# Optimization experiments

Measured on AMD Instinct MI355X. Metric: run time of the kernel, lower is better.

## Reference

```python
import jax, jax.numpy as jnp
import numpy as np

B, L, E, H = 1, 2048, 1024, 16
D = E // H
SCALE = D ** -0.5


def rotary(x):
    # x: [b, h, L, d]; ESM-style rotary over the sequence axis
    d = x.shape[-1]
    inv_freq = 1.0 / (10000.0 ** (jnp.arange(0, d, 2, dtype=jnp.float32) / d))
    t = jnp.arange(x.shape[-2], dtype=jnp.float32)
    freqs = t[:, None] * inv_freq[None, :]            # [L, d/2]
    emb = jnp.concatenate([freqs, freqs], axis=-1)    # [L, d]
    cos, sin = jnp.cos(emb), jnp.sin(emb)
    x1, x2 = jnp.split(x, 2, axis=-1)
    rot = jnp.concatenate([-x2, x1], axis=-1)
    return x * cos + rot * sin


def setup_inputs() -> dict:
    key = jax.random.key(0)
    ks = jax.random.split(key, 12)
    s = 0.02
    return {
        "query": jax.random.normal(ks[0], (B, L, E), jnp.float32),
        "key_padding_mask": jnp.zeros((B, L), dtype=bool),
        "is_same_entity": jax.random.randint(ks[1], (B, L, L), 0, 2),
        "has_same_sequence": jax.random.randint(ks[2], (B, L, L), 0, 2),
        "Wq": jax.random.normal(ks[3], (E, E), jnp.float32) * s,
        "bq": jnp.zeros((E,), jnp.float32),
        "Wk": jax.random.normal(ks[4], (E, E), jnp.float32) * s,
        "bk": jnp.zeros((E,), jnp.float32),
        "Wv": jax.random.normal(ks[5], (E, E), jnp.float32) * s,
        "bv": jnp.zeros((E,), jnp.float32),
        "Wo": jax.random.normal(ks[6], (E, E), jnp.float32) * s,
        "bo": jnp.zeros((E,), jnp.float32),
        "ent_emb": jax.random.normal(ks[7], (2, H), jnp.float32) * s,
        "seq_emb": jax.random.normal(ks[8], (2, H), jnp.float32) * s,
    }


def reference(query, key_padding_mask, is_same_entity, has_same_sequence,
              Wq, bq, Wk, bk, Wv, bv, Wo, bo, ent_emb, seq_emb):
    b, l, e = query.shape
    h, d = H, e // H

    def proj(W, bias):
        y = jnp.einsum('ble,fe->blf', query, W) + bias
        return y.reshape(b, l, h, d).transpose(0, 2, 1, 3)  # [b,h,L,d]

    q = proj(Wq, bq) * SCALE
    k = proj(Wk, bk)
    v = proj(Wv, bv)

    # pre-rotary (raw) attention weights
    attn_raw = jnp.einsum('bhid,bhjd->bhij', q, k)
    q_r, k_r = rotary(q), rotary(k)
    attn = jnp.einsum('bhid,bhjd->bhij', q_r, k_r)

    # blend: use rotary weights within same sequence, mean-shifted raw elsewhere
    hss = has_same_sequence.astype(bool)[:, None, :, :]  # [b,1,L,L]
    attn_diff = jax.lax.stop_gradient(jnp.mean(attn - attn_raw, axis=(2, 3)))  # [b,h]
    attn_raw = attn_raw + attn_diff[:, :, None, None]
    w = jnp.where(hss, attn, attn_raw)

    # learned entity/sequence positional bias
    pos = ent_emb[is_same_entity] + seq_emb[has_same_sequence]  # [b,L,L,h]
    w = w + jnp.transpose(pos, (0, 3, 1, 2))

    w = jnp.where(key_padding_mask[:, None, None, :], -jnp.inf, w)
    a = jax.nn.softmax(w, axis=-1)

    o = jnp.einsum('bhij,bhjd->bhid', a, v)
    o = o.transpose(0, 2, 1, 3).reshape(b, l, e)
    return jnp.einsum('ble,fe->blf', o, Wo) + bo
```

## Files before the change

### kernel.cpp

```cpp
#include <hip/hip_runtime.h>
#include <math.h>

constexpr int L = 2048;
constexpr int E = 1024;
constexpr int H = 16;
constexpr int D = 64;
constexpr float ATT_SCALE = 0.125f;

typedef __attribute__((ext_vector_type(8))) short short8;
typedef __attribute__((ext_vector_type(4))) float f32x4;

__device__ inline unsigned short cvt_bf16(float x) {
  unsigned int u = __builtin_bit_cast(unsigned int, x);
  unsigned int r = u + 0x7fffu + ((u >> 16) & 1u);
  return (unsigned short)(r >> 16);
}
__device__ inline short8 ld8(const unsigned short* p) {
  return *reinterpret_cast<const short8*>(p);
}

__global__ __launch_bounds__(256) void rope_table_k(float* __restrict__ cos_t,
                                                    float* __restrict__ sin_t) {
  int idx = blockIdx.x * 256 + threadIdx.x;
  if (idx >= L * 32) return;
  int l = idx >> 5, m = idx & 31;
  double invf = exp(-(double)m * (log(10000.0) / 32.0));
  double ph = (double)l * invf;
  cos_t[idx] = (float)cos(ph);
  sin_t[idx] = (float)sin(ph);
}

__global__ __launch_bounds__(256) void cvt_all_k(
    const float* __restrict__ q, const float* __restrict__ wq,
    const float* __restrict__ wk, const float* __restrict__ wv,
    const float* __restrict__ wo, unsigned short* __restrict__ dst) {
  int idx = blockIdx.x * 256 + threadIdx.x;
  const float* src;
  int local;
  if (idx < 262144)      { src = q;  local = idx; }
  else if (idx < 393216) { src = wq; local = idx - 262144; }
  else if (idx < 524288) { src = wk; local = idx - 393216; }
  else if (idx < 655360) { src = wv; local = idx - 524288; }
  else                   { src = wo; local = idx - 655360; }
  const float4* s = (const float4*)src + (size_t)local * 2;
  float4 a = s[0], b = s[1];
  short8 o;
  o[0] = cvt_bf16(a.x); o[1] = cvt_bf16(a.y); o[2] = cvt_bf16(a.z); o[3] = cvt_bf16(a.w);
  o[4] = cvt_bf16(b.x); o[5] = cvt_bf16(b.y); o[6] = cvt_bf16(b.z); o[7] = cvt_bf16(b.w);
  *(short8*)&dst[(size_t)idx * 8] = o;
}

__global__ __launch_bounds__(256) void mask_pack_k(const int* __restrict__ hss,
                                                   const int* __restrict__ ise,
                                                   unsigned char* __restrict__ mbf) {
  int idx = blockIdx.x * 256 + threadIdx.x;
  int i = idx >> 9;
  int rem = idx & 511;
  int jt = rem >> 4, lr = rem & 15;
  size_t rb = (size_t)i * 2048 + jt * 64 + lr;
  unsigned int out = 0;
#pragma unroll
  for (int c = 0; c < 4; ++c) {
    unsigned int hv = (unsigned)hss[rb + c * 16] & 1u;
    unsigned int ev = (unsigned)ise[rb + c * 16] & 1u;
    out |= (hv | (ev << 1)) << (8 * c);
  }
  *(unsigned int*)&mbf[(size_t)i * 2048 + jt * 64 + lr * 4] = out;
}

__global__ __launch_bounds__(256) void proj_qkv(
    const unsigned short* __restrict__ Xb,
    const unsigned short* __restrict__ wqb, const unsigned short* __restrict__ wkb,
    const unsigned short* __restrict__ wvb,
    const float* __restrict__ bq, const float* __restrict__ bk,
    const float* __restrict__ bv,
    float* __restrict__ qf, float* __restrict__ kf, float* __restrict__ vf) {
  int by = blockIdx.y;
  int sel = by >> 4;
  int col0 = (by & 15) * 64;
  int row0 = blockIdx.x * 64;
  const unsigned short* Wb = (sel == 0) ? wqb : (sel == 1) ? wkb : wvb;
  const float* bias = (sel == 0) ? bq : (sel == 1) ? bk : bv;
  float scale = (sel == 0) ? ATT_SCALE : 1.0f;
  float* Y = (sel == 0) ? qf : (sel == 1) ? kf : vf;

  int tid = threadIdx.x;
  int w = tid >> 6, lane = tid & 63, lr = lane & 15, lg = lane >> 4;
  int wm = w >> 1, wn = w & 1;

  f32x4 acc[2][2];
#pragma unroll
  for (int m = 0; m < 2; ++m)
#pragma unroll
    for (int n = 0; n < 2; ++n) acc[m][n] = f32x4{0.f, 0.f, 0.f, 0.f};

  const unsigned short* xa[2];
  const unsigned short* wb2[2];
#pragma unroll
  for (int m = 0; m < 2; ++m)
    xa[m] = Xb + (size_t)(row0 + wm * 32 + m * 16 + lr) * 1024 + lg * 8;
#pragma unroll
  for (int n = 0; n < 2; ++n)
    wb2[n] = Wb + (size_t)(col0 + wn * 32 + n * 16 + lr) * 1024 + lg * 8;

#pragma unroll 2
  for (int k0 = 0; k0 < 1024; k0 += 64) {
    short8 a[2][2], b[2][2];
#pragma unroll
    for (int m = 0; m < 2; ++m) {
      a[m][0] = ld8(xa[m] + k0);
      a[m][1] = ld8(xa[m] + k0 + 32);
    }
#pragma unroll
    for (int n = 0; n < 2; ++n) {
      b[n][0] = ld8(wb2[n] + k0);
      b[n][1] = ld8(wb2[n] + k0 + 32);
    }
#pragma unroll
    for (int m = 0; m < 2; ++m)
#pragma unroll
      for (int n = 0; n < 2; ++n) {
        acc[m][n] = __builtin_amdgcn_mfma_f32_16x16x32_bf16(a[m][0], b[n][0], acc[m][n], 0, 0, 0);
        acc[m][n] = __builtin_amdgcn_mfma_f32_16x16x32_bf16(a[m][1], b[n][1], acc[m][n], 0, 0, 0);
      }
  }

#pragma unroll
  for (int m = 0; m < 2; ++m)
#pragma unroll
    for (int n = 0; n < 2; ++n) {
      int f = col0 + wn * 32 + n * 16 + lr;
      float bvv = bias[f];
#pragma unroll
      for (int rr = 0; rr < 4; ++rr) {
        int row = row0 + wm * 32 + m * 16 + lg * 4 + rr;
        Y[((size_t)(f >> 6) * L + row) * 64 + (f & 63)] = (acc[m][n][rr] + bvv) * scale;
      }
    }
}

__global__ __launch_bounds__(256) void proj_o(
    const unsigned short* __restrict__ Xb, const unsigned short* __restrict__ Wb,
    const float* __restrict__ bias, float* __restrict__ out) {
  int col0 = blockIdx.y * 64;
  int row0 = blockIdx.x * 64;
  int tid = threadIdx.x;
  int w = tid >> 6, lane = tid & 63, lr = lane & 15, lg = lane >> 4;
  int wm = w >> 1, wn = w & 1;

  f32x4 acc[2][2];
#pragma unroll
  for (int m = 0; m < 2; ++m)
#pragma unroll
    for (int n = 0; n < 2; ++n) acc[m][n] = f32x4{0.f, 0.f, 0.f, 0.f};

  const unsigned short* xa[2];
  const unsigned short* wb2[2];
#pragma unroll
  for (int m = 0; m < 2; ++m)
    xa[m] = Xb + (size_t)(row0 + wm * 32 + m * 16 + lr) * 1024 + lg * 8;
#pragma unroll
  for (int n = 0; n < 2; ++n)
    wb2[n] = Wb + (size_t)(col0 + wn * 32 + n * 16 + lr) * 1024 + lg * 8;

#pragma unroll 2
  for (int k0 = 0; k0 < 1024; k0 += 64) {
    short8 a[2][2], b[2][2];
#pragma unroll
    for (int m = 0; m < 2; ++m) {
      a[m][0] = ld8(xa[m] + k0);
      a[m][1] = ld8(xa[m] + k0 + 32);
    }
#pragma unroll
    for (int n = 0; n < 2; ++n) {
      b[n][0] = ld8(wb2[n] + k0);
      b[n][1] = ld8(wb2[n] + k0 + 32);
    }
#pragma unroll
    for (int m = 0; m < 2; ++m)
#pragma unroll
      for (int n = 0; n < 2; ++n) {
        acc[m][n] = __builtin_amdgcn_mfma_f32_16x16x32_bf16(a[m][0], b[n][0], acc[m][n], 0, 0, 0);
        acc[m][n] = __builtin_amdgcn_mfma_f32_16x16x32_bf16(a[m][1], b[n][1], acc[m][n], 0, 0, 0);
      }
  }

#pragma unroll
  for (int m = 0; m < 2; ++m)
#pragma unroll
    for (int n = 0; n < 2; ++n) {
      int f = col0 + wn * 32 + n * 16 + lr;
      float bvv = bias[f];
#pragma unroll
      for (int rr = 0; rr < 4; ++rr) {
        int row = row0 + wm * 32 + m * 16 + lg * 4 + rr;
        out[(size_t)row * 1024 + f] = acc[m][n][rr] + bvv;
      }
    }
}

__global__ __launch_bounds__(256) void postproc_k(
    const float* __restrict__ q, const float* __restrict__ k,
    unsigned short* __restrict__ qb, unsigned short* __restrict__ qrb,
    unsigned short* __restrict__ kb, unsigned short* __restrict__ krb,
    const float* __restrict__ cos_t, const float* __restrict__ sin_t,
    float* __restrict__ sums) {
  int h = blockIdx.x;
  int lc = blockIdx.y;
  int t = threadIdx.x;
  int d = t & 63, lq = t >> 6;
  int m = d & 31;
  float sign = (d < 32) ? -1.0f : 1.0f;
  float sq = 0.f, sk = 0.f, sqr = 0.f, skr = 0.f;
#pragma unroll 4
  for (int i = 0; i < 16; ++i) {
    int l = lc * 64 + i * 4 + lq;
    size_t base = ((size_t)h * L + l) * 64 + d;
    float cv = cos_t[l * 32 + m], sv = sin_t[l * 32 + m];
    float qv = q[base];
    float qp = __shfl_xor(qv, 32);
    float qrv = qv * cv + sign * qp * sv;
    float kv = k[base];
    float kp = __shfl_xor(kv, 32);
    float krv = kv * cv + sign * kp * sv;
    qb[base] = cvt_bf16(qv);
    qrb[base] = cvt_bf16(qrv);
    kb[base] = cvt_bf16(kv);
    krb[base] = cvt_bf16(krv);
    sq += qv; sk += kv; sqr += qrv; skr += krv;
  }
  __shared__ float red[256];
  float vals[4] = {sq, sk, sqr, skr};
#pragma unroll
  for (int a = 0; a < 4; ++a) {
    red[t] = vals[a];
    __syncthreads();
    if (lq == 0) {
      float tot = red[d] + red[d + 64] + red[d + 128] + red[d + 192];
      atomicAdd(&sums[((size_t)a * H + h) * D + d], tot);
    }
    __syncthreads();
  }
}

__global__ __launch_bounds__(256) void vt_k(const float* __restrict__ v,
                                            unsigned short* __restrict__ vtb) {
  __shared__ float tile[64][65];
  int h = blockIdx.x, lt = blockIdx.y, t = threadIdx.x;
  int row = t >> 2, cq = (t & 3) * 16;
  const float* src = v + ((size_t)h * L + lt * 64 + row) * 64 + cq;
#pragma unroll
  for (int x = 0; x < 4; ++x) {
    float4 a = *(const float4*)&src[x * 4];
    tile[row][cq + x * 4 + 0] = a.x;
    tile[row][cq + x * 4 + 1] = a.y;
    tile[row][cq + x * 4 + 2] = a.z;
    tile[row][cq + x * 4 + 3] = a.w;
  }
  __syncthreads();
  int dcol = t >> 2, lq = (t & 3) * 16;
  short8 o0, o1;
#pragma unroll
  for (int x = 0; x < 8; ++x) o0[x] = cvt_bf16(tile[lq + x][dcol]);
#pragma unroll
  for (int x = 0; x < 8; ++x) o1[x] = cvt_bf16(tile[lq + 8 + x][dcol]);
  unsigned short* dst = vtb + ((size_t)h * 64 + dcol) * L + lt * 64 + lq;
  *(short8*)dst = o0;
  *(short8*)(dst + 8) = o1;
}

__global__ void diff_k(const float* __restrict__ sums, float* __restrict__ diffp) {
  int h = threadIdx.x;
  if (h < H) {
    const float* sq  = sums + (0 * H + h) * D;
    const float* sk  = sums + (1 * H + h) * D;
    const float* sqr = sums + (2 * H + h) * D;
    const float* skr = sums + (3 * H + h) * D;
    float a = 0.f, b = 0.f;
    for (int d = 0; d < D; ++d) { a += sqr[d] * skr[d]; b += sq[d] * sk[d]; }
    diffp[h] = (a - b) / ((float)L * (float)L);
  }
}

__global__ __launch_bounds__(256) void attn_mfma(
    const unsigned short* __restrict__ qb, const unsigned short* __restrict__ qrb,
    const unsigned short* __restrict__ kb, const unsigned short* __restrict__ krb,
    const unsigned short* __restrict__ vtb, const unsigned char* __restrict__ mbf,
    const float* __restrict__ diffp, const float* __restrict__ ent,
    const float* __restrict__ seq, float* __restrict__ opart,
    float* __restrict__ mpart, float* __restrict__ lpart) {
  __shared__ char p_s[8192];

  int bid = blockIdx.x;
  int xcd = bid & 7, g = bid >> 3;
  int h = xcd * 2 + (g >> 6);
  int sub = g & 63;
  int it = sub & 31, js = sub >> 5;
  int i0 = it * 64;
  int j0base = js * 1024;

  int tid = threadIdx.x;
  int w = tid >> 6, lane = tid & 63, lr = lane & 15, lg = lane >> 4;

  const size_t hb = (size_t)h * L * 64;
  const unsigned short* qh = qb + hb;
  const unsigned short* qrh = qrb + hb;
  const unsigned short* kh = kb + hb;
  const unsigned short* krh = krb + hb;
  const unsigned short* vth = vtb + hb;

  short8 aq[2], aqr[2];
  {
    size_t qbase = (size_t)(i0 + w * 16 + lr) * 64 + lg * 8;
    aq[0] = ld8(qh + qbase);
    aq[1] = ld8(qh + qbase + 32);
    aqr[0] = ld8(qrh + qbase);
    aqr[1] = ld8(qrh + qbase + 32);
  }

  float e0 = ent[h], de = ent[H + h] - e0;
  float s0b = seq[h], dsb = seq[H + h] - s0b;
  float base_b = e0 + s0b;
  float dh = diffp[h];

  float m_r[4], l_r[4];
  f32x4 oacc[4];
#pragma unroll
  for (int rr = 0; rr < 4; ++rr) { m_r[rr] = -INFINITY; l_r[rr] = 0.f; }
#pragma unroll
  for (int n = 0; n < 4; ++n) oacc[n] = f32x4{0.f, 0.f, 0.f, 0.f};

  int koff[4];
#pragma unroll
  for (int c = 0; c < 4; ++c) koff[c] = (c * 16 + lr) * 64 + lg * 8;
  size_t vtoff[4];
#pragma unroll
  for (int n = 0; n < 4; ++n) vtoff[n] = (size_t)(n * 16 + lr) * L + lg * 8;
  int prd0 = w * 2048 + lr * 128 + ((lg * 16) ^ ((lr & 7) << 4));
  int prd1 = w * 2048 + lr * 128 + ((64 + lg * 16) ^ ((lr & 7) << 4));
  size_t mrow0 = (size_t)(i0 + w * 16 + lg * 4) * 2048 + lr * 4;

  for (int jt = 0; jt < 16; ++jt) {
    int j0 = j0base + jt * 64;
    int jb = j0 * 64;

    f32x4 sraw[4], srot[4];
#pragma unroll
    for (int c = 0; c < 4; ++c) {
      sraw[c] = f32x4{0.f, 0.f, 0.f, 0.f};
      srot[c] = f32x4{0.f, 0.f, 0.f, 0.f};
    }
#pragma unroll
    for (int c = 0; c < 4; ++c) {
      short8 b0 = ld8(kh + jb + koff[c]);
      short8 b1 = ld8(kh + jb + koff[c] + 32);
      sraw[c] = __builtin_amdgcn_mfma_f32_16x16x32_bf16(aq[0], b0, sraw[c], 0, 0, 0);
      sraw[c] = __builtin_amdgcn_mfma_f32_16x16x32_bf16(aq[1], b1, sraw[c], 0, 0, 0);
      short8 r0 = ld8(krh + jb + koff[c]);
      short8 r1 = ld8(krh + jb + koff[c] + 32);
      srot[c] = __builtin_amdgcn_mfma_f32_16x16x32_bf16(aqr[0], r0, srot[c], 0, 0, 0);
      srot[c] = __builtin_amdgcn_mfma_f32_16x16x32_bf16(aqr[1], r1, srot[c], 0, 0, 0);
    }

    unsigned int mw[4];
#pragma unroll
    for (int rr = 0; rr < 4; ++rr)
      mw[rr] = *(const unsigned int*)(mbf + mrow0 + (size_t)rr * 2048 + j0);

#pragma unroll
    for (int rr = 0; rr < 4; ++rr) {
      float sv[4];
#pragma unroll
      for (int c = 0; c < 4; ++c) {
        unsigned int b = (mw[rr] >> (8 * c)) & 0xffu;
        float srv = sraw[c][rr] + dh;
        float sov = srot[c][rr];
        float s = ((b & 1) ? sov : srv) + base_b + ((b & 1) ? dsb : 0.f) + ((b & 2) ? de : 0.f);
        sv[c] = s;
      }
      float tmax = fmaxf(fmaxf(sv[0], sv[1]), fmaxf(sv[2], sv[3]));
#pragma unroll
      for (int off = 1; off <= 8; off <<= 1) tmax = fmaxf(tmax, __shfl_xor(tmax, off));
      float mnew = fmaxf(m_r[rr], tmax);
      float corr = __expf(m_r[rr] - mnew);
      float p[4];
      float psum = 0.f;
#pragma unroll
      for (int c = 0; c < 4; ++c) { p[c] = __expf(sv[c] - mnew); psum += p[c]; }
#pragma unroll
      for (int off = 1; off <= 8; off <<= 1) psum += __shfl_xor(psum, off);
      l_r[rr] = l_r[rr] * corr + psum;
      m_r[rr] = mnew;
#pragma unroll
      for (int n = 0; n < 4; ++n) oacc[n][rr] *= corr;
      int prow = lg * 4 + rr;
      int pb = w * 2048 + prow * 128;
      int sw = (prow & 7) << 4;
#pragma unroll
      for (int c = 0; c < 4; ++c)
        *(unsigned short*)(p_s + pb + (((c * 16 + lr) * 2) ^ sw)) = cvt_bf16(p[c]);
    }

    short8 pa0 = *(const short8*)(p_s + prd0);
    short8 pa1 = *(const short8*)(p_s + prd1);
#pragma unroll
    for (int n = 0; n < 4; ++n) {
      short8 v0 = ld8(vth + vtoff[n] + j0);
      short8 v1 = ld8(vth + vtoff[n] + j0 + 32);
      oacc[n] = __builtin_amdgcn_mfma_f32_16x16x32_bf16(pa0, v0, oacc[n], 0, 0, 0);
      oacc[n] = __builtin_amdgcn_mfma_f32_16x16x32_bf16(pa1, v1, oacc[n], 0, 0, 0);
    }
  }

#pragma unroll
  for (int rr = 0; rr < 4; ++rr) {
    int row = i0 + w * 16 + lg * 4 + rr;
    size_t pr = (size_t)(js * 16 + h) * L + row;
    size_t obase = pr * 64;
#pragma unroll
    for (int n = 0; n < 4; ++n) opart[obase + n * 16 + lr] = oacc[n][rr];
    if (lr == 0) {
      mpart[pr] = m_r[rr];
      lpart[pr] = l_r[rr];
    }
  }
}

__global__ __launch_bounds__(256) void combine_k(
    const float* __restrict__ opart, const float* __restrict__ mpart,
    const float* __restrict__ lpart, unsigned short* __restrict__ obf) {
  int idx = blockIdx.x * 256 + threadIdx.x;
  int c8 = idx & 7;
  int row = (idx >> 3) & 2047;
  int h = idx >> 14;
  size_t r0 = (size_t)h * L + row;
  size_t r1 = (size_t)(16 + h) * L + row;
  float m0 = mpart[r0], m1 = mpart[r1];
  float mm = fmaxf(m0, m1);
  float c0 = __expf(m0 - mm), c1 = __expf(m1 - mm);
  float inv = 1.0f / (lpart[r0] * c0 + lpart[r1] * c1);
  float s0 = c0 * inv, s1 = c1 * inv;
  const float4* p0 = (const float4*)&opart[r0 * 64 + c8 * 8];
  const float4* p1 = (const float4*)&opart[r1 * 64 + c8 * 8];
  float4 a0 = p0[0], a1 = p0[1], b0 = p1[0], b1 = p1[1];
  short8 o;
  o[0] = cvt_bf16(a0.x * s0 + b0.x * s1);
  o[1] = cvt_bf16(a0.y * s0 + b0.y * s1);
  o[2] = cvt_bf16(a0.z * s0 + b0.z * s1);
  o[3] = cvt_bf16(a0.w * s0 + b0.w * s1);
  o[4] = cvt_bf16(a1.x * s0 + b1.x * s1);
  o[5] = cvt_bf16(a1.y * s0 + b1.y * s1);
  o[6] = cvt_bf16(a1.z * s0 + b1.z * s1);
  o[7] = cvt_bf16(a1.w * s0 + b1.w * s1);
  *(short8*)&obf[(size_t)row * 1024 + h * 64 + c8 * 8] = o;
}

extern "C" void kernel_launch(void* const* d_in, const int* in_sizes, int n_in,
                              void* d_out, int out_size, void* d_ws, size_t ws_size,
                              hipStream_t stream) {
  (void)in_sizes; (void)n_in; (void)out_size; (void)ws_size;
  const float* query = (const float*)d_in[0];
  const int* ise = (const int*)d_in[2];
  const int* hss = (const int*)d_in[3];
  const float* Wq = (const float*)d_in[4];
  const float* bq = (const float*)d_in[5];
  const float* Wk = (const float*)d_in[6];
  const float* bk = (const float*)d_in[7];
  const float* Wv = (const float*)d_in[8];
  const float* bv = (const float*)d_in[9];
  const float* Wo = (const float*)d_in[10];
  const float* bo = (const float*)d_in[11];
  const float* ent = (const float*)d_in[12];
  const float* seq = (const float*)d_in[13];
  float* out = (float*)d_out;

  const size_t MQ = (size_t)L * E;
  const size_t MW = (size_t)E * E;

  float* ws = (float*)d_ws;
  float* qf = ws;
  float* kf = ws + MQ;
  float* vf = ws + 2 * MQ;
  float* opart = qf;
  float* mpart = vf;
  float* lpart = vf + 65536;

  unsigned short* xb  = (unsigned short*)(ws + 3 * MQ);
  unsigned short* wqb = xb + MQ;
  unsigned short* wkb = wqb + MW;
  unsigned short* wvb = wkb + MW;
  unsigned short* wob = wvb + MW;
  unsigned short* qb2 = wob + MW;
  unsigned short* qrb = qb2 + MQ;
  unsigned short* kb2 = qrb + MQ;
  unsigned short* krb = kb2 + MQ;
  unsigned short* vtb = krb + MQ;
  unsigned short* obf = vtb + MQ;

  unsigned char* mbf = (unsigned char*)(obf + MQ);
  float* tail = (float*)(mbf + (size_t)L * L);
  float* cs = tail;
  float* sn = cs + (size_t)L * 32;
  float* sums = sn + (size_t)L * 32;
  float* diffp = sums + 4096;

  rope_table_k<<<256, 256, 0, stream>>>(cs, sn);
  cvt_all_k<<<3072, 256, 0, stream>>>(query, Wq, Wk, Wv, Wo, xb);
  mask_pack_k<<<4096, 256, 0, stream>>>(hss, ise, mbf);

  proj_qkv<<<dim3(32, 48), 256, 0, stream>>>(xb, wqb, wkb, wvb, bq, bk, bv, qf, kf, vf);

  hipMemsetAsync(sums, 0, 4096 * sizeof(float), stream);
  postproc_k<<<dim3(16, 32), 256, 0, stream>>>(qf, kf, qb2, qrb, kb2, krb, cs, sn, sums);
  vt_k<<<dim3(16, 32), 256, 0, stream>>>(vf, vtb);
  diff_k<<<1, 64, 0, stream>>>(sums, diffp);

  attn_mfma<<<1024, 256, 0, stream>>>(qb2, qrb, kb2, krb, vtb, mbf, diffp, ent, seq,
                                      opart, mpart, lpart);
  combine_k<<<1024, 256, 0, stream>>>(opart, mpart, lpart, obf);

  proj_o<<<dim3(32, 16), 256, 0, stream>>>(obf, wob, bo, out);
}
```

Before: 437.0 us.

## Fuse prep kernels, enlarge QKV tiles, prefetch V and mask in attention

The three preprocessing kernels (bf16 conversion, mask packing, rope table) become one launch, and the rope/postprocess and V-transpose kernels are merged. Each QKV projection block now covers 128 rows instead of 64, halving the grid and reusing loaded weight fragments across more rows. In attention, V fragments and the next tile's mask words are loaded early, the per-row softmax sum is reduced across lanes once at the end rather than every tile, and launch bounds request 4 blocks per CU. The aim is fewer launches and more latency hiding, at the cost of higher register pressure and fewer QKV blocks.

New measurement: 502.4 us. +15.0%, slower.

```diff
diff --git a/kernel.cpp b/kernel.cpp
--- a/kernel.cpp
+++ b/kernel.cpp
@@ -19,53 +19,54 @@
   return *reinterpret_cast<const short8*>(p);
 }
 
-__global__ __launch_bounds__(256) void rope_table_k(float* __restrict__ cos_t,
-                                                    float* __restrict__ sin_t) {
-  int idx = blockIdx.x * 256 + threadIdx.x;
-  if (idx >= L * 32) return;
-  int l = idx >> 5, m = idx & 31;
-  double invf = exp(-(double)m * (log(10000.0) / 32.0));
-  double ph = (double)l * invf;
-  cos_t[idx] = (float)cos(ph);
-  sin_t[idx] = (float)sin(ph);
-}
-
-__global__ __launch_bounds__(256) void cvt_all_k(
+__global__ __launch_bounds__(256) void prep_k(
     const float* __restrict__ q, const float* __restrict__ wq,
     const float* __restrict__ wk, const float* __restrict__ wv,
-    const float* __restrict__ wo, unsigned short* __restrict__ dst) {
-  int idx = blockIdx.x * 256 + threadIdx.x;
-  const float* src;
-  int local;
-  if (idx < 262144)      { src = q;  local = idx; }
-  else if (idx < 393216) { src = wq; local = idx - 262144; }
-  else if (idx < 524288) { src = wk; local = idx - 393216; }
-  else if (idx < 655360) { src = wv; local = idx - 524288; }
-  else                   { src = wo; local = idx - 655360; }
-  const float4* s = (const float4*)src + (size_t)local * 2;
-  float4 a = s[0], b = s[1];
-  short8 o;
-  o[0] = cvt_bf16(a.x); o[1] = cvt_bf16(a.y); o[2] = cvt_bf16(a.z); o[3] = cvt_bf16(a.w);
-  o[4] = cvt_bf16(b.x); o[5] = cvt_bf16(b.y); o[6] = cvt_bf16(b.z); o[7] = cvt_bf16(b.w);
-  *(short8*)&dst[(size_t)idx * 8] = o;
-}
-
-__global__ __launch_bounds__(256) void mask_pack_k(const int* __restrict__ hss,
-                                                   const int* __restrict__ ise,
-                                                   unsigned char* __restrict__ mbf) {
-  int idx = blockIdx.x * 256 + threadIdx.x;
-  int i = idx >> 9;
-  int rem = idx & 511;
-  int jt = rem >> 4, lr = rem & 15;
-  size_t rb = (size_t)i * 2048 + jt * 64 + lr;
-  unsigned int out = 0;
-#pragma unroll
-  for (int c = 0; c < 4; ++c) {
-    unsigned int hv = (unsigned)hss[rb + c * 16] & 1u;
-    unsigned int ev = (unsigned)ise[rb + c * 16] & 1u;
-    out |= (hv | (ev << 1)) << (8 * c);
-  }
-  *(unsigned int*)&mbf[(size_t)i * 2048 + jt * 64 + lr * 4] = out;
+    const float* __restrict__ wo, unsigned short* __restrict__ dst,
+    const int* __restrict__ hss, const int* __restrict__ ise,
+    unsigned char* __restrict__ mbf,
+    float* __restrict__ cos_t, float* __restrict__ sin_t) {
+  int b = blockIdx.x;
+  int t = threadIdx.x;
+  if (b < 3072) {
+    int idx = b * 256 + t;
+    const float* src;
+    int local;
+    if (idx < 262144)      { src = q;  local = idx; }
+    else if (idx < 393216) { src = wq; local = idx - 262144; }
+    else if (idx < 524288) { src = wk; local = idx - 393216; }
+    else if (idx < 655360) { src = wv; local = idx - 524288; }
+    else                   { src = wo; local = idx - 655360; }
+    const float4* s = (const float4*)src + (size_t)local * 2;
+    float4 a = s[0], bb = s[1];
+    short8 o;
+    o[0] = cvt_bf16(a.x); o[1] = cvt_bf16(a.y); o[2] = cvt_bf16(a.z); o[3] = cvt_bf16(a.w);
+    o[4] = cvt_bf16(bb.x); o[5] = cvt_bf16(bb.y); o[6] = cvt_bf16(bb.z); o[7] = cvt_bf16(bb.w);
+    *(short8*)&dst[(size_t)idx * 8] = o;
+  } else if (b < 7168) {
+    int idx = (b - 3072) * 256 + t;
+    int i = idx >> 9;
+    int rem = idx & 511;
+    int jt = rem >> 4, lr = rem & 15;
+    size_t rb = (size_t)i * 2048 + jt * 64 + lr;
+    unsigned int out = 0;
+#pragma unroll
+    for (int c = 0; c < 4; ++c) {
+      unsigned int hv = (unsigned)hss[rb + c * 16] & 1u;
+      unsigned int ev = (unsigned)ise[rb + c * 16] & 1u;
+      out |= (hv | (ev << 1)) << (8 * c);
+    }
+    *(unsigned int*)&mbf[(size_t)i * 2048 + jt * 64 + lr * 4] = out;
+  } else {
+    int idx = (b - 7168) * 256 + t;
+    if (idx < L * 32) {
+      int l = idx >> 5, m = idx & 31;
+      double invf = exp(-(double)m * (log(10000.0) / 32.0));
+      double ph = (double)l * invf;
+      cos_t[idx] = (float)cos(ph);
+      sin_t[idx] = (float)sin(ph);
+    }
+  }
 }
 
 __global__ __launch_bounds__(256) void proj_qkv(
@@ -78,7 +79,7 @@
   int by = blockIdx.y;
   int sel = by >> 4;
   int col0 = (by & 15) * 64;
-  int row0 = blockIdx.x * 64;
+  int row0 = blockIdx.x * 128;
   const unsigned short* Wb = (sel == 0) ? wqb : (sel == 1) ? wkb : wvb;
   const float* bias = (sel == 0) ? bq : (sel == 1) ? bk : bv;
   float scale = (sel == 0) ? ATT_SCALE : 1.0f;
@@ -88,26 +89,25 @@
   int w = tid >> 6, lane = tid & 63, lr = lane & 15, lg = lane >> 4;
   int wm = w >> 1, wn = w & 1;
 
-  f32x4 acc[2][2];
-#pragma unroll
-  for (int m = 0; m < 2; ++m)
+  f32x4 acc[4][2];
+#pragma unroll
+  for (int m = 0; m < 4; ++m)
 #pragma unroll
     for (int n = 0; n < 2; ++n) acc[m][n] = f32x4{0.f, 0.f, 0.f, 0.f};
 
-  const unsigned short* xa[2];
+  const unsigned short* xa[4];
   const unsigned short* wb2[2];
 #pragma unroll
-  for (int m = 0; m < 2; ++m)
-    xa[m] = Xb + (size_t)(row0 + wm * 32 + m * 16 + lr) * 1024 + lg * 8;
+  for (int m = 0; m < 4; ++m)
+    xa[m] = Xb + (size_t)(row0 + wm * 64 + m * 16 + lr) * 1024 + lg * 8;
 #pragma unroll
   for (int n = 0; n < 2; ++n)
     wb2[n] = Wb + (size_t)(col0 + wn * 32 + n * 16 + lr) * 1024 + lg * 8;
 
-#pragma unroll 2
   for (int k0 = 0; k0 < 1024; k0 += 64) {
-    short8 a[2][2], b[2][2];
-#pragma unroll
-    for (int m = 0; m < 2; ++m) {
+    short8 a[4][2], b[2][2];
+#pragma unroll
+    for (int m = 0; m < 4; ++m) {
       a[m][0] = ld8(xa[m] + k0);
       a[m][1] = ld8(xa[m] + k0 + 32);
     }
@@ -117,7 +117,7 @@
       b[n][1] = ld8(wb2[n] + k0 + 32);
     }
 #pragma unroll
-    for (int m = 0; m < 2; ++m)
+    for (int m = 0; m < 4; ++m)
 #pragma unroll
       for (int n = 0; n < 2; ++n) {
         acc[m][n] = __builtin_amdgcn_mfma_f32_16x16x32_bf16(a[m][0], b[n][0], acc[m][n], 0, 0, 0);
@@ -126,14 +126,14 @@
   }
 
 #pragma unroll
-  for (int m = 0; m < 2; ++m)
+  for (int m = 0; m < 4; ++m)
 #pragma unroll
     for (int n = 0; n < 2; ++n) {
       int f = col0 + wn * 32 + n * 16 + lr;
       float bvv = bias[f];
 #pragma unroll
       for (int rr = 0; rr < 4; ++rr) {
-        int row = row0 + wm * 32 + m * 16 + lg * 4 + rr;
+        int row = row0 + wm * 64 + m * 16 + lg * 4 + rr;
         Y[((size_t)(f >> 6) * L + row) * 64 + (f & 63)] = (acc[m][n][rr] + bvv) * scale;
       }
     }
@@ -199,74 +199,78 @@
     }
 }
 
-__global__ __launch_bounds__(256) void postproc_k(
+__global__ __launch_bounds__(256) void postvt_k(
     const float* __restrict__ q, const float* __restrict__ k,
+    const float* __restrict__ v,
     unsigned short* __restrict__ qb, unsigned short* __restrict__ qrb,
     unsigned short* __restrict__ kb, unsigned short* __restrict__ krb,
+    unsigned short* __restrict__ vtb,
     const float* __restrict__ cos_t, const float* __restrict__ sin_t,
     float* __restrict__ sums) {
+  __shared__ float tile[64][65];
+  float* red = &tile[0][0];
+
   int h = blockIdx.x;
   int lc = blockIdx.y;
   int t = threadIdx.x;
-  int d = t & 63, lq = t >> 6;
-  int m = d & 31;
-  float sign = (d < 32) ? -1.0f : 1.0f;
-  float sq = 0.f, sk = 0.f, sqr = 0.f, skr = 0.f;
+
+  {
+    int d = t & 63, lq = t >> 6;
+    int m = d & 31;
+    float sign = (d < 32) ? -1.0f : 1.0f;
+    float sq = 0.f, sk = 0.f, sqr = 0.f, skr = 0.f;
 #pragma unroll 4
-  for (int i = 0; i < 16; ++i) {
-    int l = lc * 64 + i * 4 + lq;
-    size_t base = ((size_t)h * L + l) * 64 + d;
-    float cv = cos_t[l * 32 + m], sv = sin_t[l * 32 + m];
-    float qv = q[base];
-    float qp = __shfl_xor(qv, 32);
-    float qrv = qv * cv + sign * qp * sv;
-    float kv = k[base];
-    float kp = __shfl_xor(kv, 32);
-    float krv = kv * cv + sign * kp * sv;
-    qb[base] = cvt_bf16(qv);
-    qrb[base] = cvt_bf16(qrv);
-    kb[base] = cvt_bf16(kv);
-    krb[base] = cvt_bf16(krv);
-    sq += qv; sk += kv; sqr += qrv; skr += krv;
-  }
-  __shared__ float red[256];
-  float vals[4] = {sq, sk, sqr, skr};
-#pragma unroll
-  for (int a = 0; a < 4; ++a) {
-    red[t] = vals[a];
+    for (int i = 0; i < 16; ++i) {
+      int l = lc * 64 + i * 4 + lq;
+      size_t base = ((size_t)h * L + l) * 64 + d;
+      float cv = cos_t[l * 32 + m], sv = sin_t[l * 32 + m];
+      float qv = q[base];
+      float qp = __shfl_xor(qv, 32);
+      float qrv = qv * cv + sign * qp * sv;
+      float kv = k[base];
+      float kp = __shfl_xor(kv, 32);
+      float krv = kv * cv + sign * kp * sv;
+      qb[base] = cvt_bf16(qv);
+      qrb[base] = cvt_bf16(qrv);
+      kb[base] = cvt_bf16(kv);
+      krb[base] = cvt_bf16(krv);
+      sq += qv; sk += kv; sqr += qrv; skr += krv;
+    }
+    float vals[4] = {sq, sk, sqr, skr};
+#pragma unroll
+    for (int a = 0; a < 4; ++a) {
+      red[t] = vals[a];
+      __syncthreads();
+      if (lq == 0) {
+        float tot = red[d] + red[d + 64] + red[d + 128] + red[d + 192];
+        atomicAdd(&sums[((size_t)a * H + h) * D + d], tot);
+      }
+      __syncthreads();
+    }
+  }
+
+  {
+    int row = t >> 2, cq = (t & 3) * 16;
+    const float* src = v + ((size_t)h * L + lc * 64 + row) * 64 + cq;
+#pragma unroll
+    for (int x = 0; x < 4; ++x) {
+      float4 a = *(const float4*)&src[x * 4];
+      tile[row][cq + x * 4 + 0] = a.x;
+      tile[row][cq + x * 4 + 1] = a.y;
+      tile[row][cq + x * 4 + 2] = a.z;
+      tile[row][cq + x * 4 + 3] = a.w;
+    }
     __syncthreads();
-    if (lq == 0) {
-      float tot = red[d] + red[d + 64] + red[d + 128] + red[d + 192];
-      atomicAdd(&sums[((size_t)a * H + h) * D + d], tot);
-    }
-    __syncthreads();
-  }
-}
-
-__global__ __launch_bounds__(256) void vt_k(const float* __restrict__ v,
-                                            unsigned short* __restrict__ vtb) {
-  __shared__ float tile[64][65];
-  int h = blockIdx.x, lt = blockIdx.y, t = threadIdx.x;
-  int row = t >> 2, cq = (t & 3) * 16;
-  const float* src = v + ((size_t)h * L + lt * 64 + row) * 64 + cq;
-#pragma unroll
-  for (int x = 0; x < 4; ++x) {
-    float4 a = *(const float4*)&src[x * 4];
-    tile[row][cq + x * 4 + 0] = a.x;
-    tile[row][cq + x * 4 + 1] = a.y;
-    tile[row][cq + x * 4 + 2] = a.z;
-    tile[row][cq + x * 4 + 3] = a.w;
-  }
-  __syncthreads();
-  int dcol = t >> 2, lq = (t & 3) * 16;
-  short8 o0, o1;
-#pragma unroll
-  for (int x = 0; x < 8; ++x) o0[x] = cvt_bf16(tile[lq + x][dcol]);
-#pragma unroll
-  for (int x = 0; x < 8; ++x) o1[x] = cvt_bf16(tile[lq + 8 + x][dcol]);
-  unsigned short* dst = vtb + ((size_t)h * 64 + dcol) * L + lt * 64 + lq;
-  *(short8*)dst = o0;
-  *(short8*)(dst + 8) = o1;
+    int dcol = t >> 2, lq = (t & 3) * 16;
+    short8 o0, o1;
+#pragma unroll
+    for (int x = 0; x < 8; ++x) o0[x] = cvt_bf16(tile[lq + x][dcol]);
+#pragma unroll
+    for (int x = 0; x < 8; ++x) o1[x] = cvt_bf16(tile[lq + 8 + x][dcol]);
+    unsigned short* dst = vtb + ((size_t)h * 64 + dcol) * L + lc * 64 + lq;
+    *(short8*)dst = o0;
+    *(short8*)(dst + 8) = o1;
+  }
 }
 
 __global__ void diff_k(const float* __restrict__ sums, float* __restrict__ diffp) {
@@ -282,7 +286,7 @@
   }
 }
 
-__global__ __launch_bounds__(256) void attn_mfma(
+__global__ __launch_bounds__(256, 4) void attn_mfma(
     const unsigned short* __restrict__ qb, const unsigned short* __restrict__ qrb,
     const unsigned short* __restrict__ kb, const unsigned short* __restrict__ krb,
     const unsigned short* __restrict__ vtb, const unsigned char* __restrict__ mbf,
@@ -340,9 +344,21 @@
   int prd1 = w * 2048 + lr * 128 + ((64 + lg * 16) ^ ((lr & 7) << 4));
   size_t mrow0 = (size_t)(i0 + w * 16 + lg * 4) * 2048 + lr * 4;
 
+  unsigned int mw[4];
+#pragma unroll
+  for (int rr = 0; rr < 4; ++rr)
+    mw[rr] = *(const unsigned int*)(mbf + mrow0 + (size_t)rr * 2048 + j0base);
+
   for (int jt = 0; jt < 16; ++jt) {
     int j0 = j0base + jt * 64;
     int jb = j0 * 64;
+
+    short8 v0[4], v1[4];
+#pragma unroll
+    for (int n = 0; n < 4; ++n) {
+      v0[n] = ld8(vth + vtoff[n] + j0);
+      v1[n] = ld8(vth + vtoff[n] + j0 + 32);
+    }
 
     f32x4 sraw[4], srot[4];
 #pragma unroll
@@ -362,10 +378,12 @@
       srot[c] = __builtin_amdgcn_mfma_f32_16x16x32_bf16(aqr[1], r1, srot[c], 0, 0, 0);
     }
 
-    unsigned int mw[4];
-#pragma unroll
-    for (int rr = 0; rr < 4; ++rr)
-      mw[rr] = *(const unsigned int*)(mbf + mrow0 + (size_t)rr * 2048 + j0);
+    unsigned int mwn[4] = {0u, 0u, 0u, 0u};
+    if (jt < 15) {
+#pragma unroll
+      for (int rr = 0; rr < 4; ++rr)
+        mwn[rr] = *(const unsigned int*)(mbf + mrow0 + (size_t)rr * 2048 + j0 + 64);
+    }
 
 #pragma unroll
     for (int rr = 0; rr < 4; ++rr) {
@@ -383,37 +401,39 @@
       for (int off = 1; off <= 8; off <<= 1) tmax = fmaxf(tmax, __shfl_xor(tmax, off));
       float mnew = fmaxf(m_r[rr], tmax);
       float corr = __expf(m_r[rr] - mnew);
-      float p[4];
-      float psum = 0.f;
-#pragma unroll
-      for (int c = 0; c < 4; ++c) { p[c] = __expf(sv[c] - mnew); psum += p[c]; }
-#pragma unroll
-      for (int off = 1; off <= 8; off <<= 1) psum += __shfl_xor(psum, off);
-      l_r[rr] = l_r[rr] * corr + psum;
-      m_r[rr] = mnew;
-#pragma unroll
-      for (int n = 0; n < 4; ++n) oacc[n][rr] *= corr;
+      float lacc = 0.f;
       int prow = lg * 4 + rr;
       int pb = w * 2048 + prow * 128;
       int sw = (prow & 7) << 4;
 #pragma unroll
-      for (int c = 0; c < 4; ++c)
-        *(unsigned short*)(p_s + pb + (((c * 16 + lr) * 2) ^ sw)) = cvt_bf16(p[c]);
+      for (int c = 0; c < 4; ++c) {
+        float p = __expf(sv[c] - mnew);
+        lacc += p;
+        *(unsigned short*)(p_s + pb + (((c * 16 + lr) * 2) ^ sw)) = cvt_bf16(p);
+      }
+      l_r[rr] = l_r[rr] * corr + lacc;
+      m_r[rr] = mnew;
+#pragma unroll
+      for (int n = 0; n < 4; ++n) oacc[n][rr] *= corr;
     }
 
     short8 pa0 = *(const short8*)(p_s + prd0);
     short8 pa1 = *(const short8*)(p_s + prd1);
 #pragma unroll
     for (int n = 0; n < 4; ++n) {
-      short8 v0 = ld8(vth + vtoff[n] + j0);
-      short8 v1 = ld8(vth + vtoff[n] + j0 + 32);
-      oacc[n] = __builtin_amdgcn_mfma_f32_16x16x32_bf16(pa0, v0, oacc[n], 0, 0, 0);
-      oacc[n] = __builtin_amdgcn_mfma_f32_16x16x32_bf16(pa1, v1, oacc[n], 0, 0, 0);
-    }
+      oacc[n] = __builtin_amdgcn_mfma_f32_16x16x32_bf16(pa0, v0[n], oacc[n], 0, 0, 0);
+      oacc[n] = __builtin_amdgcn_mfma_f32_16x16x32_bf16(pa1, v1[n], oacc[n], 0, 0, 0);
+    }
+
+#pragma unroll
+    for (int rr = 0; rr < 4; ++rr) mw[rr] = mwn[rr];
   }
 
 #pragma unroll
   for (int rr = 0; rr < 4; ++rr) {
+    float lsum = l_r[rr];
+#pragma unroll
+    for (int off = 1; off <= 8; off <<= 1) lsum += __shfl_xor(lsum, off);
     int row = i0 + w * 16 + lg * 4 + rr;
     size_t pr = (size_t)(js * 16 + h) * L + row;
     size_t obase = pr * 64;
@@ -421,7 +441,7 @@
     for (int n = 0; n < 4; ++n) opart[obase + n * 16 + lr] = oacc[n][rr];
     if (lr == 0) {
       mpart[pr] = m_r[rr];
-      lpart[pr] = l_r[rr];
+      lpart[pr] = lsum;
     }
   }
 }
@@ -504,15 +524,13 @@
   float* sums = sn + (size_t)L * 32;
   float* diffp = sums + 4096;
 
-  rope_table_k<<<256, 256, 0, stream>>>(cs, sn);
-  cvt_all_k<<<3072, 256, 0, stream>>>(query, Wq, Wk, Wv, Wo, xb);
-  mask_pack_k<<<4096, 256, 0, stream>>>(hss, ise, mbf);
-
-  proj_qkv<<<dim3(32, 48), 256, 0, stream>>>(xb, wqb, wkb, wvb, bq, bk, bv, qf, kf, vf);
-
+  prep_k<<<7424, 256, 0, stream>>>(query, Wq, Wk, Wv, Wo, xb, hss, ise, mbf, cs, sn);
   hipMemsetAsync(sums, 0, 4096 * sizeof(float), stream);
-  postproc_k<<<dim3(16, 32), 256, 0, stream>>>(qf, kf, qb2, qrb, kb2, krb, cs, sn, sums);
-  vt_k<<<dim3(16, 32), 256, 0, stream>>>(vf, vtb);
+
+  proj_qkv<<<dim3(16, 48), 256, 0, stream>>>(xb, wqb, wkb, wvb, bq, bk, bv, qf, kf, vf);
+
+  postvt_k<<<dim3(16, 32), 256, 0, stream>>>(qf, kf, vf, qb2, qrb, kb2, krb, vtb,
+                                             cs, sn, sums);
   diff_k<<<1, 64, 0, stream>>>(sums, diffp);
 
   attn_mfma<<<1024, 256, 0, stream>>>(qb2, qrb, kb2, krb, vtb, mbf, diffp, ent, seq,
```
